# Performance work log

Measured on AMD Instinct MI355X. Metric: run time of the kernel, lower is better.

Reference implementation:

```python
import jax, jax.numpy as jnp
import numpy as np

B, C, H, W = 4, 64, 64, 64
E = 64            # embed_dim
K_TOP = 128       # k (init arg), K_TOP <= N
N = H * W


def conv2d(x, w, b, pad):
    # x: [B,C,H,W], w: [O,I,kh,kw]
    y = jax.lax.conv_general_dilated(
        x, w, window_strides=(1, 1), padding=[(pad, pad), (pad, pad)],
        dimension_numbers=('NCHW', 'OIHW', 'NCHW'))
    return y + b[None, :, None, None]


def setup_inputs() -> dict:
    key = jax.random.key(0)
    ks = jax.random.split(key, 16)
    def w_init(k, shape, fan_in):
        return jax.random.normal(k, shape, jnp.float32) * (1.0 / np.sqrt(fan_in))
    return {
        'x':  jax.random.normal(ks[0], (B, C, H, W), jnp.float32),
        'w1': w_init(ks[1], (C, C, 1, 1), C),
        'b1': jnp.zeros((C,), jnp.float32),
        'w3': w_init(ks[2], (C, C, 3, 3), C * 9),
        'b3': jnp.zeros((C,), jnp.float32),
        'w5': w_init(ks[3], (C, C, 5, 5), C * 25),
        'b5': jnp.zeros((C,), jnp.float32),
        'wq': w_init(ks[4], (3 * C, E), 3 * C),
        'bq': jnp.zeros((E,), jnp.float32),
        'wk': w_init(ks[5], (3 * C, E), 3 * C),
        'bk': jnp.zeros((E,), jnp.float32),
        'wv': w_init(ks[6], (3 * C, C), 3 * C),
        'bv': jnp.zeros((C,), jnp.float32),
        'wo': w_init(ks[7], (C, C), C),
        'bo': jnp.zeros((C,), jnp.float32),
    }


def reference(x, w1, b1, w3, b3, w5, b5, wq, bq, wk, bk, wv, bv, wo, bo):
    b, c, h, w = x.shape
    n = h * w
    # multi-scale conv paths
    f1 = conv2d(x, w1, b1, 0)
    f2 = conv2d(x, w3, b3, 1)
    f3 = conv2d(x, w5, b5, 2)
    f_multi = jnp.concatenate([f1, f2, f3], axis=1)          # [B,3C,H,W]
    f_flat = f_multi.reshape(b, 3 * c, n).transpose(0, 2, 1)  # [B,N,3C]
    Q = f_flat @ wq + bq                                      # [B,N,E]
    Kt = f_flat @ wk + bk                                     # [B,N,E]
    V = f_flat @ wv + bv                                      # [B,N,C]
    attn = jnp.einsum('bqe,bke->bqk', Q, Kt) / np.sqrt(E)     # [B,N,N]
    attn = jax.nn.softmax(attn, axis=-1)
    key_importance = attn.sum(axis=1)                         # [B,N]
    _, topk_idx = jax.lax.top_k(key_importance, K_TOP)        # [B,K]
    mask = jnp.zeros_like(key_importance)
    mask = mask.at[jnp.arange(b)[:, None], topk_idx].set(1.0)  # [B,N]
    out = jnp.einsum('bqk,bkc->bqc', attn * mask[:, None, :], V)  # [B,N,C]
    out = out @ wo + bo
    return out.transpose(0, 2, 1).reshape(b, c, h, w)
```

## Files before the change

kernel.cpp:

```cpp
#include <hip/hip_runtime.h>
#include <math.h>

#define N_PIX 4096
#define CCH 64

typedef __attribute__((ext_vector_type(8))) short short8;
typedef __attribute__((ext_vector_type(4))) float f32x4;
typedef __attribute__((ext_vector_type(16))) float f32x16;

#define EXP2C 0.18033688f

__device__ __forceinline__ int swz(int row, int col) {
  return row * 68 + (col ^ (((row >> 2) & 7) << 2));
}

__device__ __forceinline__ float fget(const float4& v, int j) {
  return ((const float*)&v)[j];
}

__device__ __forceinline__ unsigned short f2bf(float f) {
  unsigned u = __float_as_uint(f);
  unsigned r = (u + 0x7fff + ((u >> 16) & 1)) >> 16;
  return (unsigned short)r;
}
__device__ __forceinline__ float bf2f(unsigned short h) {
  return __uint_as_float((unsigned)h << 16);
}

__device__ __forceinline__ float fexp2(float x) {
#if __has_builtin(__builtin_amdgcn_exp2f)
  return __builtin_amdgcn_exp2f(x);
#else
  return exp2f(x);
#endif
}

__device__ __forceinline__ void gll16(const unsigned short* g, unsigned short* lbase,
                                      int lane) {
#if __has_builtin(__builtin_amdgcn_global_load_lds)
  (void)lane;
  __builtin_amdgcn_global_load_lds(
      (const __attribute__((address_space(1))) void*)g,
      (__attribute__((address_space(3))) void*)lbase, 16, 0, 0);
#else
  *(short8*)(lbase + lane * 8) = *(const short8*)g;
#endif
}

__global__ __launch_bounds__(256) void prep_kernel(
    const float* __restrict__ w1, const float* __restrict__ w3,
    const float* __restrict__ w5, const float* __restrict__ wq,
    const float* __restrict__ wk, const float* __restrict__ wv,
    const float* __restrict__ b1, const float* __restrict__ b3,
    const float* __restrict__ b5, const float* __restrict__ bq,
    const float* __restrict__ bk, const float* __restrict__ bv,
    unsigned short* __restrict__ Bfh, unsigned short* __restrict__ Bfl,
    float* __restrict__ beff) {
  __shared__ float At[64 * 68];
  __shared__ float Bt[64 * 68];
  const int which = blockIdx.x, t = blockIdx.y;
  const float* Wsel = which == 0 ? wq : (which == 1 ? wk : wv);
  const int tid = threadIdx.x, tx = tid & 15, ty = tid >> 4;
  if (t == 25) {
    if (tid < 64) {
      const float* bsel = which == 0 ? bq : (which == 1 ? bk : bv);
      float s = bsel[tid];
      for (int row = 0; row < 192; ++row) {
        const float bc = row < 64 ? b1[row] : (row < 128 ? b3[row - 64] : b5[row - 128]);
        s += bc * Wsel[row * 64 + tid];
      }
      beff[which * 64 + tid] = s;
    }
    return;
  }
  const int ky = t / 5, kx = t % 5;
  const bool in3 = (ky >= 1 && ky <= 3 && kx >= 1 && kx <= 3);
  const bool c1 = (t == 12);
  const int t3 = (ky - 1) * 3 + (kx - 1);
  float acc[4][4];
#pragma unroll
  for (int i = 0; i < 4; ++i)
#pragma unroll
    for (int j = 0; j < 4; ++j) acc[i][j] = 0.f;
  const int npass = 1 + (in3 ? 1 : 0) + (c1 ? 1 : 0);
  for (int pass = 0; pass < npass; ++pass) {
    const int kind = pass == 0 ? 0 : (pass == 1 && in3 ? 1 : 2);
    const int rowbase = kind == 0 ? 128 : (kind == 1 ? 64 : 0);
    __syncthreads();
    for (int v = tid; v < 4096; v += 256) {
      const int i = v & 63, o = v >> 6;
      float a;
      if (kind == 0) a = w5[(size_t)(o * 64 + i) * 25 + t];
      else if (kind == 1) a = w3[(size_t)(o * 64 + i) * 9 + t3];
      else a = w1[o * 64 + i];
      At[swz(i, o)] = a;
    }
    for (int v = tid; v < 1024; v += 256) {
      const int row = v >> 4, c4 = (v & 15) * 4;
      *(float4*)&Bt[swz(row, c4)] = *(const float4*)(Wsel + (rowbase + row) * 64 + c4);
    }
    __syncthreads();
#pragma unroll
    for (int o4 = 0; o4 < 16; ++o4) {
      float4 a[4], b[4];
#pragma unroll
      for (int i = 0; i < 4; ++i) a[i] = *(const float4*)&At[swz(ty * 4 + i, o4 * 4)];
#pragma unroll
      for (int u = 0; u < 4; ++u) b[u] = *(const float4*)&Bt[swz(o4 * 4 + u, tx * 4)];
#pragma unroll
      for (int i = 0; i < 4; ++i)
#pragma unroll
        for (int j = 0; j < 4; ++j)
#pragma unroll
          for (int u = 0; u < 4; ++u)
            acc[i][j] = fmaf(fget(a[i], u), fget(b[u], j), acc[i][j]);
    }
  }
#pragma unroll
  for (int ii = 0; ii < 4; ++ii) {
    const int i = ty * 4 + ii;
    const int s = i >> 5, lg = (i >> 3) & 3, j = i & 7;
#pragma unroll
    for (int jj = 0; jj < 4; ++jj) {
      const int em = tx * 4 + jj;
      const int q = which * 4 + (em >> 4), lr = em & 15;
      const size_t off = ((size_t)(t * 12 + q) * 2 + s) * 512 + (lg * 16 + lr) * 8 + j;
      const float val = acc[ii][jj];
      const unsigned short h = f2bf(val);
      Bfh[off] = h;
      Bfl[off] = f2bf(val - bf2f(h));
    }
  }
}

__global__ __launch_bounds__(256) void xpose_kernel(const float* __restrict__ x,
                                                    unsigned short* __restrict__ Xth,
                                                    unsigned short* __restrict__ Xtl) {
  __shared__ float t[64][65];
  const int yp = blockIdx.x;
  const int b = blockIdx.y;
  const int tid = threadIdx.x;
  const size_t rowbase = ((size_t)b * 68 + yp) * 72 * 64;
  short8 z8 = {0, 0, 0, 0, 0, 0, 0, 0};
  if (yp < 2 || yp >= 66) {
    short8* ph = (short8*)(Xth + rowbase);
    short8* pl = (short8*)(Xtl + rowbase);
    for (int v = tid; v < 576; v += 256) {
      ph[v] = z8;
      pl[v] = z8;
    }
    return;
  }
  const int y = yp - 2;
  for (int it = 0; it < 16; ++it) {
    const int v = it * 256 + tid;
    const int c = v >> 6, xx = v & 63;
    t[xx][c] = x[(((size_t)b * 64 + c) * 64 + y) * 64 + xx];
  }
  for (int s = tid; s < 64; s += 256) {
    const int col = s >> 3;
    const int xp = col < 2 ? col : col + 64;
    const size_t o = rowbase + (size_t)xp * 64 + (s & 7) * 8;
    *(short8*)(Xth + o) = z8;
    *(short8*)(Xtl + o) = z8;
  }
  __syncthreads();
  for (int it = 0; it < 16; ++it) {
    const int v = it * 256 + tid;
    const int xx = v >> 6, c = v & 63;
    const float val = t[xx][c];
    const unsigned short h = f2bf(val);
    const unsigned short lo = f2bf(val - bf2f(h));
    const int xp = xx + 2;
    const size_t idx = rowbase + (size_t)xp * 64 + (c ^ ((xp & 7) << 3));
    Xth[idx] = h;
    Xtl[idx] = lo;
  }
}

__global__ __launch_bounds__(256) void fused_qkv_kernel(
    const unsigned short* __restrict__ Xth, const unsigned short* __restrict__ Xtl,
    const unsigned short* __restrict__ Bfh, const unsigned short* __restrict__ Bfl,
    const float* __restrict__ beff, unsigned short* __restrict__ Qhi,
    unsigned short* __restrict__ Qlo, unsigned short* __restrict__ Khi,
    unsigned short* __restrict__ Klo, float* __restrict__ Vm) {
  __shared__ unsigned short Lh[192 * 64];
  __shared__ unsigned short Ll[192 * 64];
  const int b = blockIdx.y, sb = blockIdx.x;
  const int y0 = (sb >> 3) * 8, x0 = (sb & 7) * 8;
  const int tid = threadIdx.x, wv = tid >> 6, l = tid & 63;
  const int lr = l & 15, lg = l >> 4;
  const int qd = blockIdx.z * 4 + wv;
#pragma unroll
  for (int rr = 0; rr < 3; ++rr) {
    const int py = wv * 3 + rr;
    const size_t src = (((size_t)b * 68 + y0 + py) * 72 + x0) * 64 + (size_t)l * 8;
    gll16(Xth + src, &Lh[py * 1024], l);
    gll16(Xth + src + 512, &Lh[py * 1024 + 512], l);
    gll16(Xtl + src, &Ll[py * 1024], l);
    gll16(Xtl + src + 512, &Ll[py * 1024 + 512], l);
  }
  __syncthreads();
  f32x4 acc[4];
#pragma unroll
  for (int pg = 0; pg < 4; ++pg) acc[pg] = (f32x4){0.f, 0.f, 0.f, 0.f};
  for (int ky = 0; ky < 5; ++ky) {
    for (int kx = 0; kx < 5; ++kx) {
      const int t = ky * 5 + kx;
      const size_t f = ((size_t)(t * 12 + qd)) * 2;
      const short8 bh0 = *(const short8*)&Bfh[f * 512 + l * 8];
      const short8 bh1 = *(const short8*)&Bfh[(f + 1) * 512 + l * 8];
      const short8 bl0 = *(const short8*)&Bfl[f * 512 + l * 8];
      const short8 bl1 = *(const short8*)&Bfl[(f + 1) * 512 + l * 8];
#pragma unroll
      for (int pg = 0; pg < 4; ++pg) {
        const int p = pg * 16 + lr;
        const int prt = ((p >> 3) + ky) * 16 + (p & 7) + kx;
        const int rb = prt * 64, sw = (prt & 7) << 3;
        const short8 ah0 = *(const short8*)&Lh[rb + ((lg * 8) ^ sw)];
        const short8 ah1 = *(const short8*)&Lh[rb + ((32 + lg * 8) ^ sw)];
        const short8 al0 = *(const short8*)&Ll[rb + ((lg * 8) ^ sw)];
        const short8 al1 = *(const short8*)&Ll[rb + ((32 + lg * 8) ^ sw)];
        acc[pg] = __builtin_amdgcn_mfma_f32_16x16x32_bf16(ah0, bh0, acc[pg], 0, 0, 0);
        acc[pg] = __builtin_amdgcn_mfma_f32_16x16x32_bf16(ah1, bh1, acc[pg], 0, 0, 0);
        acc[pg] = __builtin_amdgcn_mfma_f32_16x16x32_bf16(al0, bh0, acc[pg], 0, 0, 0);
        acc[pg] = __builtin_amdgcn_mfma_f32_16x16x32_bf16(al1, bh1, acc[pg], 0, 0, 0);
        acc[pg] = __builtin_amdgcn_mfma_f32_16x16x32_bf16(ah0, bl0, acc[pg], 0, 0, 0);
        acc[pg] = __builtin_amdgcn_mfma_f32_16x16x32_bf16(ah1, bl1, acc[pg], 0, 0, 0);
      }
    }
  }
  const size_t base = (size_t)b * N_PIX;
  {
    const int e = qd * 16 + lr;
    const int which = e >> 6, em = e & 63;
    const float be = beff[e];
#pragma unroll
    for (int pg = 0; pg < 4; ++pg) {
#pragma unroll
      for (int r = 0; r < 4; ++r) {
        const int pp = pg * 16 + lg * 4 + r;
        const int n = (y0 + (pp >> 3)) * 64 + x0 + (pp & 7);
        const float val = acc[pg][r] + be;
        const size_t off = (base + n) * 64 + em;
        if (which == 2) {
          Vm[off] = val;
        } else {
          const unsigned short h = f2bf(val);
          const unsigned short lo = f2bf(val - bf2f(h));
          if (which == 0) {
            Qhi[off] = h;
            Qlo[off] = lo;
          } else {
            Khi[off] = h;
            Klo[off] = lo;
          }
        }
      }
    }
  }
}

__global__ __launch_bounds__(256) void qk_s_kernel(
    const unsigned short* __restrict__ Qhi, const unsigned short* __restrict__ Qlo,
    const unsigned short* __restrict__ Khi, const unsigned short* __restrict__ Klo,
    float* __restrict__ s_part) {
  __shared__ unsigned short Kst[2][2][2048];
  const int b = blockIdx.z, kc = blockIdx.y, q0 = blockIdx.x * 128;
  const int tid = threadIdx.x, wv = tid >> 6, l = tid & 63;
  const int lr = l & 31, lh = l >> 5;
  const size_t base = (size_t)b * N_PIX;
  const size_t qoff = (base + q0 + wv * 32 + lr) * 64 + lh * 8;
  short8 qh[4], ql[4];
#pragma unroll
  for (int f = 0; f < 4; ++f) {
    qh[f] = *(const short8*)(Qhi + qoff + f * 16);
    ql[f] = *(const short8*)(Qlo + qoff + f * 16);
  }
  const int srow = tid >> 3;
  const int gcu = ((tid & 7) * 8) ^ ((srow & 7) << 3);
  const unsigned short* Ksh = Khi + (base + kc * 512 + srow) * 64 + gcu;
  const unsigned short* Ksl = Klo + (base + kc * 512 + srow) * 64 + gcu;
  float racc[16];
#pragma unroll
  for (int r = 0; r < 16; ++r) racc[r] = 0.f;

#define STAGE(bb, t)                                   \
  {                                                    \
    const size_t go_ = (size_t)(t) * 2048;             \
    gll16(Ksh + go_, &Kst[bb][0][wv * 512], l);        \
    gll16(Ksl + go_, &Kst[bb][1][wv * 512], l);        \
  }
#define COMP(bb)                                                                     \
  {                                                                                  \
    short8 kh_[4], kl_[4];                                                           \
    const int rb_ = lr * 64, sw_ = (lr & 7) << 3;                                    \
    _Pragma("unroll") for (int f = 0; f < 4; ++f) {                                  \
      const int c_ = rb_ + ((lh * 8 + f * 16) ^ sw_);                                \
      kh_[f] = *(const short8*)&Kst[bb][0][c_];                                      \
      kl_[f] = *(const short8*)&Kst[bb][1][c_];                                      \
    }                                                                                \
    f32x16 a0, a1;                                                                   \
    _Pragma("unroll") for (int r = 0; r < 16; ++r) { a0[r] = 0.f; a1[r] = 0.f; }     \
    a0 = __builtin_amdgcn_mfma_f32_32x32x16_bf16(qh[0], kh_[0], a0, 0, 0, 0);        \
    a1 = __builtin_amdgcn_mfma_f32_32x32x16_bf16(qh[2], kh_[2], a1, 0, 0, 0);        \
    a0 = __builtin_amdgcn_mfma_f32_32x32x16_bf16(qh[1], kh_[1], a0, 0, 0, 0);        \
    a1 = __builtin_amdgcn_mfma_f32_32x32x16_bf16(qh[3], kh_[3], a1, 0, 0, 0);        \
    a0 = __builtin_amdgcn_mfma_f32_32x32x16_bf16(ql[0], kh_[0], a0, 0, 0, 0);        \
    a1 = __builtin_amdgcn_mfma_f32_32x32x16_bf16(ql[2], kh_[2], a1, 0, 0, 0);        \
    a0 = __builtin_amdgcn_mfma_f32_32x32x16_bf16(ql[1], kh_[1], a0, 0, 0, 0);        \
    a1 = __builtin_amdgcn_mfma_f32_32x32x16_bf16(ql[3], kh_[3], a1, 0, 0, 0);        \
    a0 = __builtin_amdgcn_mfma_f32_32x32x16_bf16(qh[0], kl_[0], a0, 0, 0, 0);        \
    a1 = __builtin_amdgcn_mfma_f32_32x32x16_bf16(qh[2], kl_[2], a1, 0, 0, 0);        \
    a0 = __builtin_amdgcn_mfma_f32_32x32x16_bf16(qh[1], kl_[1], a0, 0, 0, 0);        \
    a1 = __builtin_amdgcn_mfma_f32_32x32x16_bf16(qh[3], kl_[3], a1, 0, 0, 0);        \
    _Pragma("unroll") for (int r = 0; r < 16; ++r)                                   \
        racc[r] += fexp2((a0[r] + a1[r]) * EXP2C);                                   \
  }

  STAGE(0, 0);
  __syncthreads();
  int bu = 0;
  for (int t = 0; t < 16; ++t) {
    if (t < 15) STAGE(bu ^ 1, t + 1);
    COMP(bu);
    __syncthreads();
    bu ^= 1;
  }
#undef STAGE
#undef COMP
#pragma unroll
  for (int r = 0; r < 16; ++r)
#pragma unroll
    for (int m = 1; m < 32; m <<= 1) racc[r] += __shfl_xor(racc[r], m);
  if (lr == 0) {
#pragma unroll
    for (int r = 0; r < 16; ++r) {
      const int row = (r & 3) + 8 * (r >> 2) + 4 * lh;
      s_part[((size_t)(b * 8 + kc) << 12) + q0 + wv * 32 + row] = racc[r];
    }
  }
}

__global__ __launch_bounds__(256) void combine_kernel(const float* __restrict__ s_part,
                                                      float* __restrict__ invs,
                                                      float* __restrict__ lg2w) {
  const int g = blockIdx.x * 256 + threadIdx.x;
  const int b = g >> 12, q = g & 4095;
  float s = 0.f;
#pragma unroll
  for (int kc = 0; kc < 8; ++kc) s += s_part[((size_t)(b * 8 + kc) << 12) + q];
  invs[g] = 1.f / s;
  lg2w[g] = -__log2f(s);
}

__global__ __launch_bounds__(256) void colsum_kernel2(
    const unsigned short* __restrict__ Qhi, const unsigned short* __restrict__ Qlo,
    const unsigned short* __restrict__ Khi, const unsigned short* __restrict__ Klo,
    const float* __restrict__ lg2w, float* __restrict__ cs_part) {
  __shared__ unsigned short Qst[2][2][2048];
  const int b = blockIdx.z, qc = blockIdx.y, k0 = blockIdx.x * 128;
  const int tid = threadIdx.x, wv = tid >> 6, l = tid & 63;
  const int lr = l & 31, lh = l >> 5;
  const size_t base = (size_t)b * N_PIX;
  const size_t koff = (base + k0 + wv * 32 + lr) * 64 + lh * 8;
  short8 kh[4], kl[4];
#pragma unroll
  for (int f = 0; f < 4; ++f) {
    kh[f] = *(const short8*)(Khi + koff + f * 16);
    kl[f] = *(const short8*)(Klo + koff + f * 16);
  }
  const int srow = tid >> 3;
  const int gcu = ((tid & 7) * 8) ^ ((srow & 7) << 3);
  const unsigned short* Qsh = Qhi + (base + qc * 512 + srow) * 64 + gcu;
  const unsigned short* Qsl = Qlo + (base + qc * 512 + srow) * 64 + gcu;
  const float* lwp = lg2w + b * N_PIX + qc * 512 + lr;
  float kacc[16];
#pragma unroll
  for (int r = 0; r < 16; ++r) kacc[r] = 0.f;

#define STAGE(bb, t)                                   \
  {                                                    \
    const size_t go_ = (size_t)(t) * 2048;             \
    gll16(Qsh + go_, &Qst[bb][0][wv * 512], l);        \
    gll16(Qsl + go_, &Qst[bb][1][wv * 512], l);        \
  }
#define COMP(bb, lw_)                                                                \
  {                                                                                  \
    short8 qh_[4], ql_[4];                                                           \
    const int rb_ = lr * 64, sw_ = (lr & 7) << 3;                                    \
    _Pragma("unroll") for (int f = 0; f < 4; ++f) {                                  \
      const int c_ = rb_ + ((lh * 8 + f * 16) ^ sw_);                                \
      qh_[f] = *(const short8*)&Qst[bb][0][c_];                                      \
      ql_[f] = *(const short8*)&Qst[bb][1][c_];                                      \
    }                                                                                \
    f32x16 a0, a1;                                                                   \
    _Pragma("unroll") for (int r = 0; r < 16; ++r) { a0[r] = 0.f; a1[r] = 0.f; }     \
    a0 = __builtin_amdgcn_mfma_f32_32x32x16_bf16(kh[0], qh_[0], a0, 0, 0, 0);        \
    a1 = __builtin_amdgcn_mfma_f32_32x32x16_bf16(kh[2], qh_[2], a1, 0, 0, 0);        \
    a0 = __builtin_amdgcn_mfma_f32_32x32x16_bf16(kh[1], qh_[1], a0, 0, 0, 0);        \
    a1 = __builtin_amdgcn_mfma_f32_32x32x16_bf16(kh[3], qh_[3], a1, 0, 0, 0);        \
    a0 = __builtin_amdgcn_mfma_f32_32x32x16_bf16(kl[0], qh_[0], a0, 0, 0, 0);        \
    a1 = __builtin_amdgcn_mfma_f32_32x32x16_bf16(kl[2], qh_[2], a1, 0, 0, 0);        \
    a0 = __builtin_amdgcn_mfma_f32_32x32x16_bf16(kl[1], qh_[1], a0, 0, 0, 0);        \
    a1 = __builtin_amdgcn_mfma_f32_32x32x16_bf16(kl[3], qh_[3], a1, 0, 0, 0);        \
    a0 = __builtin_amdgcn_mfma_f32_32x32x16_bf16(kh[0], ql_[0], a0, 0, 0, 0);        \
    a1 = __builtin_amdgcn_mfma_f32_32x32x16_bf16(kh[2], ql_[2], a1, 0, 0, 0);        \
    a0 = __builtin_amdgcn_mfma_f32_32x32x16_bf16(kh[1], ql_[1], a0, 0, 0, 0);        \
    a1 = __builtin_amdgcn_mfma_f32_32x32x16_bf16(kh[3], ql_[3], a1, 0, 0, 0);        \
    _Pragma("unroll") for (int r = 0; r < 16; ++r)                                   \
        kacc[r] += fexp2(fmaf(a0[r] + a1[r], EXP2C, lw_));                           \
  }

  STAGE(0, 0);
  float lwa = lwp[0], lwb;
  __syncthreads();
  int bu = 0;
  for (int t = 0; t < 16; ++t) {
    if (t < 15) {
      STAGE(bu ^ 1, t + 1);
      lwb = lwp[(t + 1) * 32];
    }
    COMP(bu, lwa);
    lwa = lwb;
    __syncthreads();
    bu ^= 1;
  }
#undef STAGE
#undef COMP
#pragma unroll
  for (int r = 0; r < 16; ++r)
#pragma unroll
    for (int m = 1; m < 32; m <<= 1) kacc[r] += __shfl_xor(kacc[r], m);
  if (lr == 0) {
#pragma unroll
    for (int r = 0; r < 16; ++r) {
      const int row = (r & 3) + 8 * (r >> 2) + 4 * lh;
      cs_part[((size_t)(b * 8 + qc) << 12) + k0 + wv * 32 + row] = kacc[r];
    }
  }
}

__global__ __launch_bounds__(256) void topk_kernel(const float* __restrict__ cs_part,
                                                   int* __restrict__ topk) {
  __shared__ unsigned keys[4096];
  __shared__ unsigned hist[256];
  __shared__ unsigned sbuf[256];
  __shared__ unsigned selB, selNeed;
  const int b = blockIdx.x, tid = threadIdx.x;
  for (int v = tid; v < 4096; v += 256) {
    float s = 0.f;
#pragma unroll
    for (int qc = 0; qc < 8; ++qc) s += cs_part[((size_t)(b * 8 + qc) << 12) + v];
    unsigned u = __float_as_uint(s);
    keys[v] = (u & 0x80000000u) ? ~u : (u | 0x80000000u);
  }
  unsigned need = 128, prefix = 0;
  __syncthreads();
  for (int d = 3; d >= 0; --d) {
    const int shift = d * 8;
    hist[tid] = 0;
    __syncthreads();
    for (int v = tid; v < 4096; v += 256) {
      const unsigned k = keys[v];
      if (d == 3 || (k >> (shift + 8)) == prefix)
        atomicAdd(&hist[(k >> shift) & 255], 1u);
    }
    __syncthreads();
    sbuf[tid] = hist[tid];
    __syncthreads();
    for (int off = 1; off < 256; off <<= 1) {
      const unsigned add = (tid + off < 256) ? sbuf[tid + off] : 0;
      __syncthreads();
      sbuf[tid] += add;
      __syncthreads();
    }
    const unsigned sufGe = sbuf[tid];
    const unsigned sufGt = (tid < 255) ? sbuf[tid + 1] : 0;
    if (sufGt < need && need <= sufGe) {
      selB = (unsigned)tid;
      selNeed = need - sufGt;
    }
    __syncthreads();
    prefix = (prefix << 8) | selB;
    need = selNeed;
    __syncthreads();
  }
  const unsigned T = prefix;
  unsigned gtc = 0, eqc = 0;
#pragma unroll
  for (int j = 0; j < 16; ++j) {
    const unsigned k = keys[tid * 16 + j];
    gtc += (k > T);
    eqc += (k == T);
  }
  sbuf[tid] = (gtc << 16) | eqc;
  __syncthreads();
  for (int off = 1; off < 256; off <<= 1) {
    const unsigned add = (tid >= off) ? sbuf[tid - off] : 0;
    __syncthreads();
    sbuf[tid] += add;
    __syncthreads();
  }
  const unsigned incl = sbuf[tid];
  const unsigned gBase = (incl >> 16) - gtc;
  const unsigned eBase = (incl & 0xffffu) - eqc;
  const unsigned nGt = sbuf[255] >> 16;
  unsigned g = 0, e = 0;
#pragma unroll
  for (int j = 0; j < 16; ++j) {
    const int idx = tid * 16 + j;
    const unsigned k = keys[idx];
    if (k > T) {
      topk[b * 128 + gBase + g] = idx;
      ++g;
    } else if (k == T) {
      if (eBase + e < need) topk[b * 128 + nGt + eBase + e] = idx;
      ++e;
    }
  }
}

__global__ __launch_bounds__(256) void attn_out_kernel(
    const unsigned short* __restrict__ Qhp, const unsigned short* __restrict__ Qlp,
    const unsigned short* __restrict__ Khp, const unsigned short* __restrict__ Klp,
    const float* __restrict__ Vm, const float* __restrict__ invs,
    const int* __restrict__ topkb, const float* __restrict__ wo,
    const float* __restrict__ bo, float* __restrict__ dout) {
  __shared__ float Qld[32 * 68], Kld[64 * 68], Vt[64 * 68], Pl[32 * 68], Wl[64 * 68];
  __shared__ int sidx[64];
  const int b = blockIdx.y, q0 = blockIdx.x * 32;
  const int tid = threadIdx.x, tx = tid & 15, ty = tid >> 4;
  const size_t base = (size_t)b * N_PIX;
  for (int v = tid; v < 512; v += 256) {
    int row = v >> 4, c4 = (v & 15) * 4;
    size_t off = (base + q0 + row) * 64 + c4;
    ushort4 h = *(const ushort4*)(Qhp + off);
    ushort4 lo = *(const ushort4*)(Qlp + off);
    float4 f;
    f.x = bf2f(h.x) + bf2f(lo.x);
    f.y = bf2f(h.y) + bf2f(lo.y);
    f.z = bf2f(h.z) + bf2f(lo.z);
    f.w = bf2f(h.w) + bf2f(lo.w);
    *(float4*)&Qld[swz(row, c4)] = f;
  }
  for (int v = tid; v < 1024; v += 256) {
    int row = v >> 4, c4 = (v & 15) * 4;
    *(float4*)&Wl[swz(row, c4)] = *(const float4*)(wo + row * 64 + c4);
  }
  float is[2];
#pragma unroll
  for (int i = 0; i < 2; ++i) is[i] = invs[base + q0 + ty * 2 + i];
  float acc[2][4];
#pragma unroll
  for (int i = 0; i < 2; ++i)
#pragma unroll
    for (int j = 0; j < 4; ++j) acc[i][j] = 0.f;
  for (int ch = 0; ch < 2; ++ch) {
    __syncthreads();
    if (tid < 64) sidx[tid] = topkb[b * 128 + ch * 64 + tid];
    __syncthreads();
    for (int v = tid; v < 1024; v += 256) {
      int row = v >> 4, c4 = (v & 15) * 4;
      size_t off = (base + sidx[row]) * 64 + c4;
      ushort4 h = *(const ushort4*)(Khp + off);
      ushort4 lo = *(const ushort4*)(Klp + off);
      float4 f;
      f.x = bf2f(h.x) + bf2f(lo.x);
      f.y = bf2f(h.y) + bf2f(lo.y);
      f.z = bf2f(h.z) + bf2f(lo.z);
      f.w = bf2f(h.w) + bf2f(lo.w);
      *(float4*)&Kld[swz(row, c4)] = f;
    }
    for (int v = tid; v < 4096; v += 256) {
      int row = v >> 6, c = v & 63;
      Vt[swz(c, row)] = Vm[(base + sidx[row]) * 64 + c];
    }
    __syncthreads();
    float z[2][4];
#pragma unroll
    for (int i = 0; i < 2; ++i)
#pragma unroll
      for (int j = 0; j < 4; ++j) z[i][j] = 0.f;
#pragma unroll
    for (int e4 = 0; e4 < 16; ++e4) {
      float4 qa[2], ka[4];
#pragma unroll
      for (int i = 0; i < 2; ++i) qa[i] = *(const float4*)&Qld[swz(ty * 2 + i, e4 * 4)];
#pragma unroll
      for (int j = 0; j < 4; ++j) ka[j] = *(const float4*)&Kld[swz(tx * 4 + j, e4 * 4)];
#pragma unroll
      for (int i = 0; i < 2; ++i)
#pragma unroll
        for (int j = 0; j < 4; ++j)
#pragma unroll
          for (int u = 0; u < 4; ++u)
            z[i][j] = fmaf(fget(qa[i], u), fget(ka[j], u), z[i][j]);
    }
#pragma unroll
    for (int i = 0; i < 2; ++i)
#pragma unroll
      for (int j = 0; j < 4; ++j)
        Pl[swz(ty * 2 + i, tx * 4 + j)] = __expf(z[i][j] * 0.125f) * is[i];
    __syncthreads();
#pragma unroll
    for (int k4 = 0; k4 < 16; ++k4) {
      float4 pr[2], vr[4];
#pragma unroll
      for (int i = 0; i < 2; ++i) pr[i] = *(const float4*)&Pl[swz(ty * 2 + i, k4 * 4)];
#pragma unroll
      for (int j = 0; j < 4; ++j) vr[j] = *(const float4*)&Vt[swz(tx * 4 + j, k4 * 4)];
#pragma unroll
      for (int i = 0; i < 2; ++i)
#pragma unroll
        for (int j = 0; j < 4; ++j)
#pragma unroll
          for (int u = 0; u < 4; ++u)
            acc[i][j] = fmaf(fget(pr[i], u), fget(vr[j], u), acc[i][j]);
    }
  }
  __syncthreads();
#pragma unroll
  for (int i = 0; i < 2; ++i)
#pragma unroll
    for (int j = 0; j < 4; ++j) Pl[swz(ty * 2 + i, tx * 4 + j)] = acc[i][j];
  __syncthreads();
  float yacc[2][4];
#pragma unroll
  for (int i = 0; i < 2; ++i)
#pragma unroll
    for (int j = 0; j < 4; ++j) yacc[i][j] = 0.f;
#pragma unroll
  for (int e4 = 0; e4 < 16; ++e4) {
    float4 a[2], wr[4];
#pragma unroll
    for (int i = 0; i < 2; ++i) a[i] = *(const float4*)&Pl[swz(ty * 2 + i, e4 * 4)];
#pragma unroll
    for (int u = 0; u < 4; ++u) wr[u] = *(const float4*)&Wl[swz(e4 * 4 + u, tx * 4)];
#pragma unroll
    for (int i = 0; i < 2; ++i)
#pragma unroll
      for (int j = 0; j < 4; ++j)
#pragma unroll
        for (int u = 0; u < 4; ++u)
          yacc[i][j] = fmaf(fget(a[i], u), fget(wr[u], j), yacc[i][j]);
  }
  __syncthreads();
#pragma unroll
  for (int i = 0; i < 2; ++i)
#pragma unroll
    for (int j = 0; j < 4; ++j)
      Qld[swz(ty * 2 + i, tx * 4 + j)] = yacc[i][j] + bo[tx * 4 + j];
  __syncthreads();
  for (int v = tid; v < 2048; v += 256) {
    int c = v >> 5, nl = v & 31;
    dout[((size_t)b * 64 + c) * 4096 + q0 + nl] = Qld[swz(nl, c)];
  }
}

extern "C" void kernel_launch(void* const* d_in, const int* in_sizes, int n_in,
                              void* d_out, int out_size, void* d_ws, size_t ws_size,
                              hipStream_t stream) {
  const float* x = (const float*)d_in[0];
  const float* w1 = (const float*)d_in[1];
  const float* b1 = (const float*)d_in[2];
  const float* w3 = (const float*)d_in[3];
  const float* b3 = (const float*)d_in[4];
  const float* w5 = (const float*)d_in[5];
  const float* b5 = (const float*)d_in[6];
  const float* wq = (const float*)d_in[7];
  const float* bq = (const float*)d_in[8];
  const float* wk = (const float*)d_in[9];
  const float* bk = (const float*)d_in[10];
  const float* wv = (const float*)d_in[11];
  const float* bv = (const float*)d_in[12];
  const float* wo = (const float*)d_in[13];
  const float* bo = (const float*)d_in[14];

  const size_t BN = (size_t)4 * N_PIX;
  char* p = (char*)d_ws;
  auto carve = [&](size_t bytes) -> void* {
    void* r = (void*)p;
    p += (bytes + 255) & ~(size_t)255;
    return r;
  };
  unsigned short* Bfh = (unsigned short*)carve((size_t)25 * 12 * 2 * 512 * 2);
  unsigned short* Bfl = (unsigned short*)carve((size_t)25 * 12 * 2 * 512 * 2);
  float* beff = (float*)carve(192 * 4);
  unsigned short* Xth = (unsigned short*)carve((size_t)4 * 68 * 72 * 64 * 2);
  unsigned short* Xtl = (unsigned short*)carve((size_t)4 * 68 * 72 * 64 * 2);
  float* Vm = (float*)carve(BN * 64 * 4);
  unsigned short* Qhi = (unsigned short*)carve(BN * 64 * 2);
  unsigned short* Qlo = (unsigned short*)carve(BN * 64 * 2);
  unsigned short* Khi = (unsigned short*)carve(BN * 64 * 2);
  unsigned short* Klo = (unsigned short*)carve(BN * 64 * 2);
  float* s_part = (float*)carve((size_t)4 * 8 * 4096 * 4);
  float* invs = (float*)carve(BN * 4);
  float* lg2w = (float*)carve(BN * 4);
  float* cs_part = (float*)carve((size_t)4 * 8 * 4096 * 4);
  int* topkbuf = (int*)carve(512 * 4);

  prep_kernel<<<dim3(3, 26), 256, 0, stream>>>(w1, w3, w5, wq, wk, wv, b1, b3, b5,
                                               bq, bk, bv, Bfh, Bfl, beff);
  xpose_kernel<<<dim3(68, 4), 256, 0, stream>>>(x, Xth, Xtl);
  fused_qkv_kernel<<<dim3(64, 4, 3), 256, 0, stream>>>(Xth, Xtl, Bfh, Bfl, beff, Qhi,
                                                       Qlo, Khi, Klo, Vm);
  qk_s_kernel<<<dim3(32, 8, 4), 256, 0, stream>>>(Qhi, Qlo, Khi, Klo, s_part);
  combine_kernel<<<64, 256, 0, stream>>>(s_part, invs, lg2w);
  colsum_kernel2<<<dim3(32, 8, 4), 256, 0, stream>>>(Qhi, Qlo, Khi, Klo, lg2w, cs_part);
  topk_kernel<<<4, 256, 0, stream>>>(cs_part, topkbuf);
  attn_out_kernel<<<dim3(128, 4), 256, 0, stream>>>(Qhi, Qlo, Khi, Klo, Vm, invs,
                                                    topkbuf, wo, bo, (float*)d_out);
}
```

Before: 159.0 us.

## Split QK row-sum and column-sum over 16 chunks and fold combine into colsum

The qk_s and colsum kernels now split the key/query dimension into 16 chunks of 256 instead of 8 chunks of 512. This doubles the grid from 1024 to 2048 blocks, each running half as many pipeline stages. The separate combine kernel is removed: each colsum block sums the 16 row-sum partials for its 256 queries, keeps the log2 weights in shared memory, and x-block 0 writes invs. The cost is twice as many partial buffers to write and reduce, plus redundant partial-sum reads across all 32 x-blocks.

```diff
diff --git a/kernel.cpp b/kernel.cpp
--- a/kernel.cpp
+++ b/kernel.cpp
@@ -279,8 +279,8 @@
   }
   const int srow = tid >> 3;
   const int gcu = ((tid & 7) * 8) ^ ((srow & 7) << 3);
-  const unsigned short* Ksh = Khi + (base + kc * 512 + srow) * 64 + gcu;
-  const unsigned short* Ksl = Klo + (base + kc * 512 + srow) * 64 + gcu;
+  const unsigned short* Ksh = Khi + (base + kc * 256 + srow) * 64 + gcu;
+  const unsigned short* Ksl = Klo + (base + kc * 256 + srow) * 64 + gcu;
   float racc[16];
 #pragma unroll
   for (int r = 0; r < 16; ++r) racc[r] = 0.f;
@@ -321,8 +321,8 @@
   STAGE(0, 0);
   __syncthreads();
   int bu = 0;
-  for (int t = 0; t < 16; ++t) {
-    if (t < 15) STAGE(bu ^ 1, t + 1);
+  for (int t = 0; t < 8; ++t) {
+    if (t < 7) STAGE(bu ^ 1, t + 1);
     COMP(bu);
     __syncthreads();
     bu ^= 1;
@@ -337,28 +337,18 @@
 #pragma unroll
     for (int r = 0; r < 16; ++r) {
       const int row = (r & 3) + 8 * (r >> 2) + 4 * lh;
-      s_part[((size_t)(b * 8 + kc) << 12) + q0 + wv * 32 + row] = racc[r];
-    }
-  }
-}
-
-__global__ __launch_bounds__(256) void combine_kernel(const float* __restrict__ s_part,
-                                                      float* __restrict__ invs,
-                                                      float* __restrict__ lg2w) {
-  const int g = blockIdx.x * 256 + threadIdx.x;
-  const int b = g >> 12, q = g & 4095;
-  float s = 0.f;
-#pragma unroll
-  for (int kc = 0; kc < 8; ++kc) s += s_part[((size_t)(b * 8 + kc) << 12) + q];
-  invs[g] = 1.f / s;
-  lg2w[g] = -__log2f(s);
+      s_part[((size_t)(b * 16 + kc) << 12) + q0 + wv * 32 + row] = racc[r];
+    }
+  }
 }
 
 __global__ __launch_bounds__(256) void colsum_kernel2(
     const unsigned short* __restrict__ Qhi, const unsigned short* __restrict__ Qlo,
     const unsigned short* __restrict__ Khi, const unsigned short* __restrict__ Klo,
-    const float* __restrict__ lg2w, float* __restrict__ cs_part) {
+    const float* __restrict__ s_part, float* __restrict__ invs,
+    float* __restrict__ cs_part) {
   __shared__ unsigned short Qst[2][2][2048];
+  __shared__ float lg2wl[256];
   const int b = blockIdx.z, qc = blockIdx.y, k0 = blockIdx.x * 128;
   const int tid = threadIdx.x, wv = tid >> 6, l = tid & 63;
   const int lr = l & 31, lh = l >> 5;
@@ -372,9 +362,8 @@
   }
   const int srow = tid >> 3;
   const int gcu = ((tid & 7) * 8) ^ ((srow & 7) << 3);
-  const unsigned short* Qsh = Qhi + (base + qc * 512 + srow) * 64 + gcu;
-  const unsigned short* Qsl = Qlo + (base + qc * 512 + srow) * 64 + gcu;
-  const float* lwp = lg2w + b * N_PIX + qc * 512 + lr;
+  const unsigned short* Qsh = Qhi + (base + qc * 256 + srow) * 64 + gcu;
+  const unsigned short* Qsl = Qlo + (base + qc * 256 + srow) * 64 + gcu;
   float kacc[16];
 #pragma unroll
   for (int r = 0; r < 16; ++r) kacc[r] = 0.f;
@@ -385,8 +374,9 @@
     gll16(Qsh + go_, &Qst[bb][0][wv * 512], l);        \
     gll16(Qsl + go_, &Qst[bb][1][wv * 512], l);        \
   }
-#define COMP(bb, lw_)                                                                \
+#define COMP(bb, t_)                                                                 \
   {                                                                                  \
+    const float lw_ = lg2wl[(t_) * 32 + lr];                                         \
     short8 qh_[4], ql_[4];                                                           \
     const int rb_ = lr * 64, sw_ = (lr & 7) << 3;                                    \
     _Pragma("unroll") for (int f = 0; f < 4; ++f) {                                  \
@@ -413,16 +403,19 @@
   }
 
   STAGE(0, 0);
-  float lwa = lwp[0], lwb;
+  {
+    const int q = qc * 256 + tid;
+    float s = 0.f;
+#pragma unroll
+    for (int c = 0; c < 16; ++c) s += s_part[((size_t)(b * 16 + c) << 12) + q];
+    lg2wl[tid] = -__log2f(s);
+    if (blockIdx.x == 0) invs[b * N_PIX + q] = 1.f / s;
+  }
   __syncthreads();
   int bu = 0;
-  for (int t = 0; t < 16; ++t) {
-    if (t < 15) {
-      STAGE(bu ^ 1, t + 1);
-      lwb = lwp[(t + 1) * 32];
-    }
-    COMP(bu, lwa);
-    lwa = lwb;
+  for (int t = 0; t < 8; ++t) {
+    if (t < 7) STAGE(bu ^ 1, t + 1);
+    COMP(bu, t);
     __syncthreads();
     bu ^= 1;
   }
@@ -436,7 +429,7 @@
 #pragma unroll
     for (int r = 0; r < 16; ++r) {
       const int row = (r & 3) + 8 * (r >> 2) + 4 * lh;
-      cs_part[((size_t)(b * 8 + qc) << 12) + k0 + wv * 32 + row] = kacc[r];
+      cs_part[((size_t)(b * 16 + qc) << 12) + k0 + wv * 32 + row] = kacc[r];
     }
   }
 }
@@ -451,7 +444,7 @@
   for (int v = tid; v < 4096; v += 256) {
     float s = 0.f;
 #pragma unroll
-    for (int qc = 0; qc < 8; ++qc) s += cs_part[((size_t)(b * 8 + qc) << 12) + v];
+    for (int qc = 0; qc < 16; ++qc) s += cs_part[((size_t)(b * 16 + qc) << 12) + v];
     unsigned u = __float_as_uint(s);
     keys[v] = (u & 0x80000000u) ? ~u : (u | 0x80000000u);
   }
@@ -694,10 +687,9 @@
   unsigned short* Qlo = (unsigned short*)carve(BN * 64 * 2);
   unsigned short* Khi = (unsigned short*)carve(BN * 64 * 2);
   unsigned short* Klo = (unsigned short*)carve(BN * 64 * 2);
-  float* s_part = (float*)carve((size_t)4 * 8 * 4096 * 4);
+  float* s_part = (float*)carve((size_t)4 * 16 * 4096 * 4);
   float* invs = (float*)carve(BN * 4);
-  float* lg2w = (float*)carve(BN * 4);
-  float* cs_part = (float*)carve((size_t)4 * 8 * 4096 * 4);
+  float* cs_part = (float*)carve((size_t)4 * 16 * 4096 * 4);
   int* topkbuf = (int*)carve(512 * 4);
 
   prep_kernel<<<dim3(3, 26), 256, 0, stream>>>(w1, w3, w5, wq, wk, wv, b1, b3, b5,
@@ -705,9 +697,9 @@
   xpose_kernel<<<dim3(68, 4), 256, 0, stream>>>(x, Xth, Xtl);
   fused_qkv_kernel<<<dim3(64, 4, 3), 256, 0, stream>>>(Xth, Xtl, Bfh, Bfl, beff, Qhi,
                                                        Qlo, Khi, Klo, Vm);
-  qk_s_kernel<<<dim3(32, 8, 4), 256, 0, stream>>>(Qhi, Qlo, Khi, Klo, s_part);
-  combine_kernel<<<64, 256, 0, stream>>>(s_part, invs, lg2w);
-  colsum_kernel2<<<dim3(32, 8, 4), 256, 0, stream>>>(Qhi, Qlo, Khi, Klo, lg2w, cs_part);
+  qk_s_kernel<<<dim3(32, 16, 4), 256, 0, stream>>>(Qhi, Qlo, Khi, Klo, s_part);
+  colsum_kernel2<<<dim3(32, 16, 4), 256, 0, stream>>>(Qhi, Qlo, Khi, Klo, s_part,
+                                                      invs, cs_part);
   topk_kernel<<<4, 256, 0, stream>>>(cs_part, topkbuf);
   attn_out_kernel<<<dim3(128, 4), 256, 0, stream>>>(Qhi, Qlo, Khi, Klo, Vm, invs,
                                                     topkbuf, wo, bo, (float*)d_out);
```

Result: slower. 168.9 us (+6.2%).
